# Kernel optimization log

Measured on AMD Instinct MI355X. Metric: run time of the kernel, lower is better.

## Reference

```python
import jax, jax.numpy as jnp
import numpy as np

B, C, H, W = 8, 64, 160, 160
N_HEADS = 8
EPS = 1e-6


def conv1x1(x, w, b):
    # x: [B, Cin, H, W], w: [Cout, Cin], b: [Cout]
    return jnp.einsum('oc,bchw->bohw', w, x) + b[None, :, None, None]


def setup_inputs() -> dict:
    key = jax.random.key(0)
    ks = jax.random.split(key, 12)
    s = 0.05
    return {
        'high': jax.random.normal(ks[0], (B, C, H, W), jnp.float32),
        'low': jax.random.normal(ks[1], (B, C, H, W), jnp.float32),
        'wq_high': jax.random.normal(ks[2], (C // 2, C), jnp.float32) * s,
        'bq_high': jnp.zeros((C // 2,), jnp.float32),
        'wq_low': jax.random.normal(ks[3], (C // 2, C), jnp.float32) * s,
        'bq_low': jnp.zeros((C // 2,), jnp.float32),
        'wk': jax.random.normal(ks[4], (C, C), jnp.float32) * s,
        'bk': jnp.zeros((C,), jnp.float32),
        'wv': jax.random.normal(ks[5], (C, C), jnp.float32) * s,
        'bv': jnp.zeros((C,), jnp.float32),
        'wo': jax.random.normal(ks[6], (C, C), jnp.float32) * s,
        'bo': jnp.zeros((C,), jnp.float32),
    }


def reference(high, low, wq_high, bq_high, wq_low, bq_low, wk, bk, wv, bv, wo, bo):
    b, c, h, w = low.shape
    p, d, n = N_HEADS, c // N_HEADS, h * w
    # q branches: [B, C//2, H, W] -> [B, P/2, N, d]
    hq = conv1x1(high, wq_high, bq_high).reshape(b, p // 2, d, n).transpose(0, 1, 3, 2)
    lq = conv1x1(low, wq_low, bq_low).reshape(b, p // 2, d, n).transpose(0, 1, 3, 2)
    q = jax.nn.softplus(jnp.concatenate([hq, lq], axis=1))          # [B, P, N, d]
    k = jax.nn.softplus(conv1x1(low, wk, bk).reshape(b, p, d, n))   # [B, P, d, N]
    v = conv1x1(low, wv, bv).reshape(b, p, d, n)                    # [B, P, d, N]
    # linear-attention context: kT v over spatial N
    attn_map = jnp.einsum('bpmn,bpcn->bpmc', k, v)                  # [B, P, d, d]
    norm = 1.0 / jnp.einsum('bpnc,bpc->bpn', q, jnp.sum(k, axis=-1) + EPS)  # [B, P, N]
    out = jnp.einsum('bpnm,bpmc,bpn->bpcn', q, attn_map, norm)      # [B, P, d, N]
    out = out.reshape(b, c, h, w)
    return conv1x1(out, wo, bo)
```

## Files before the change

kernel.cpp:

```cpp
#include <hip/hip_runtime.h>

#define NPIX  25600
#define NB    8
#define NCH   200
#define KPX   128
#define EPSV  1e-6f

#define WS_WKVT  0
#define WS_WQT   8192
#define WS_BKV   12288
#define WS_BQ    12416
#define WS_PART  12480
#define WS_G     934080
#define WS_KSE   966848
#define WS_WKVM  966912
#define WS_BKVM  975104

typedef __attribute__((ext_vector_type(8))) short short8v;
typedef __attribute__((ext_vector_type(4))) float f32x4v;

__device__ __forceinline__ unsigned short f2bf(float x) {
  unsigned u = __float_as_uint(x);
  return (unsigned short)((u + 0x7FFFu + ((u >> 16) & 1u)) >> 16);
}
__device__ __forceinline__ float bf2f(unsigned short h) {
  return __uint_as_float(((unsigned)h) << 16);
}

__device__ __forceinline__ float softplus_(float x) {
  return (x > 20.0f) ? x : __logf(1.0f + __expf(x));
}

__global__ void k0_pack(const float* __restrict__ wq_high, const float* __restrict__ bq_high,
                        const float* __restrict__ wq_low,  const float* __restrict__ bq_low,
                        const float* __restrict__ wk, const float* __restrict__ bk,
                        const float* __restrict__ wv, const float* __restrict__ bv,
                        float* __restrict__ ws) {
  const int tid = threadIdx.x;
  for (int e = tid; e < 4096; e += 256) {
    int m = e & 7, c = (e >> 3) & 63, h = e >> 9;
    float v = (h < 4) ? wq_high[(h * 8 + m) * 64 + c]
                      : wq_low[((h - 4) * 8 + m) * 64 + c];
    ws[WS_WQT + e] = v;
  }
  for (int e = tid; e < 64; e += 256) {
    int m = e & 7, h = e >> 3;
    ws[WS_BQ + e] = (h < 4) ? bq_high[h * 8 + m] : bq_low[(h - 4) * 8 + m];
  }
  unsigned short* wmp = (unsigned short*)(ws + WS_WKVM);
  for (int e = tid; e < 16384; e += 256) {
    int j = e & 7, l = (e >> 3) & 63, frag = e >> 9;
    int sp = frag & 1, ks = (frag >> 1) & 1, mt = frag >> 2;
    int row = l & 15, k32 = (l >> 4) * 8 + j, c = ks * 32 + k32;
    int head = (mt & 3) * 2 + (row >> 3), m = row & 7;
    float wv_ = (mt < 4) ? wk[(head * 8 + m) * 64 + c] : wv[(head * 8 + m) * 64 + c];
    unsigned short hb = f2bf(wv_);
    wmp[e] = (sp == 0) ? hb : f2bf(wv_ - bf2f(hb));
  }
  for (int e = tid; e < 128; e += 256) {
    int mt = e >> 4, row = e & 15;
    int head = (mt & 3) * 2 + (row >> 3), m = row & 7;
    ws[WS_BKVM + e] = (mt < 4) ? bk[head * 8 + m] : bv[head * 8 + m];
  }
}

__global__ __attribute__((amdgpu_waves_per_eu(1, 8)))
void k1_kv(const float* __restrict__ low,
           const float* __restrict__ ws,
           float* __restrict__ part) {
  const int b = blockIdx.y, chunk = blockIdx.x;
  const int tid = threadIdx.x, lane = tid & 63;
  const int w = __builtin_amdgcn_readfirstlane(tid >> 6);
  const int l15 = lane & 15, lg = lane >> 4;
  __shared__ float kvL[16384];
  const float* lowb = low + (size_t)b * 64 * NPIX + chunk * KPX + w * 32;
  short8v xhi[2][2], xlo[2][2];
#pragma unroll
  for (int nt = 0; nt < 2; nt++)
#pragma unroll
    for (int ks = 0; ks < 2; ks++) {
      const float* xp = lowb + (size_t)(ks * 32 + lg * 8) * NPIX + nt * 16 + l15;
      float xs[8];
#pragma unroll
      for (int j = 0; j < 8; j++) xs[j] = xp[(size_t)j * NPIX];
#pragma unroll
      for (int j = 0; j < 8; j++) {
        unsigned short h = f2bf(xs[j]);
        xhi[nt][ks][j] = (short)h;
        xlo[nt][ks][j] = (short)f2bf(xs[j] - bf2f(h));
      }
    }
  const unsigned short* wm = (const unsigned short*)(ws + WS_WKVM);
  const float* bm = ws + WS_BKVM;
#pragma unroll
  for (int mt = 0; mt < 8; mt++) {
    f32x4v a0 = {0.f, 0.f, 0.f, 0.f}, a1 = {0.f, 0.f, 0.f, 0.f};
#pragma unroll
    for (int ks = 0; ks < 2; ks++) {
      short8v whi = *(const short8v*)(wm + (((mt * 4 + ks * 2 + 0) * 64) + lane) * 8);
      short8v wlo = *(const short8v*)(wm + (((mt * 4 + ks * 2 + 1) * 64) + lane) * 8);
      a0 = __builtin_amdgcn_mfma_f32_16x16x32_bf16(whi, xhi[0][ks], a0, 0, 0, 0);
      a0 = __builtin_amdgcn_mfma_f32_16x16x32_bf16(whi, xlo[0][ks], a0, 0, 0, 0);
      a0 = __builtin_amdgcn_mfma_f32_16x16x32_bf16(wlo, xhi[0][ks], a0, 0, 0, 0);
      a1 = __builtin_amdgcn_mfma_f32_16x16x32_bf16(whi, xhi[1][ks], a1, 0, 0, 0);
      a1 = __builtin_amdgcn_mfma_f32_16x16x32_bf16(whi, xlo[1][ks], a1, 0, 0, 0);
      a1 = __builtin_amdgcn_mfma_f32_16x16x32_bf16(wlo, xhi[1][ks], a1, 0, 0, 0);
    }
#pragma unroll
    for (int r = 0; r < 4; r++) {
      const int row = mt * 16 + lg * 4 + r;
      const float bb = bm[row];
      float v0 = a0[r] + bb, v1 = a1[r] + bb;
      if (mt < 4) { v0 = softplus_(v0); v1 = softplus_(v1); }
      const int px0 = w * 32 + l15, px1 = w * 32 + 16 + l15;
      kvL[row * 128 + ((((px0 >> 2) ^ (row & 7))) << 2) + (px0 & 3)] = v0;
      kvL[row * 128 + ((((px1 >> 2) ^ (row & 7))) << 2) + (px1 & 3)] = v1;
    }
  }
  __syncthreads();
  const int col = l15;
#pragma unroll
  for (int hh = 0; hh < 2; hh++) {
    const int h = w + hh * 4;
    f32x4v acc = {0.f, 0.f, 0.f, 0.f};
    const int arow = h * 8 + (l15 & 7);
    const int brow = 64 + h * 8 + (col < 8 ? col : 0);
#pragma unroll
    for (int ks = 0; ks < 4; ks++) {
      const int pxl = ks * 32 + lg * 8;
      const int sA = arow & 7;
      float4 af0 = *(const float4*)&kvL[arow * 128 + (((pxl >> 2) ^ sA) << 2)];
      float4 af1 = *(const float4*)&kvL[arow * 128 + ((((pxl >> 2) + 1) ^ sA) << 2)];
      float as[8] = {af0.x, af0.y, af0.z, af0.w, af1.x, af1.y, af1.z, af1.w};
      float bs[8];
      if (col < 8) {
        const int sB = brow & 7;
        float4 bf0 = *(const float4*)&kvL[brow * 128 + (((pxl >> 2) ^ sB) << 2)];
        float4 bf1 = *(const float4*)&kvL[brow * 128 + ((((pxl >> 2) + 1) ^ sB) << 2)];
        bs[0]=bf0.x; bs[1]=bf0.y; bs[2]=bf0.z; bs[3]=bf0.w;
        bs[4]=bf1.x; bs[5]=bf1.y; bs[6]=bf1.z; bs[7]=bf1.w;
      } else {
        const float fill = (col == 8) ? 1.0f : 0.0f;
#pragma unroll
        for (int j = 0; j < 8; j++) bs[j] = fill;
      }
      short8v ahi, alo, bhi, blo;
#pragma unroll
      for (int j = 0; j < 8; j++) {
        unsigned short ha = f2bf(as[j]);
        ahi[j] = (short)ha; alo[j] = (short)f2bf(as[j] - bf2f(ha));
        unsigned short hb = f2bf(bs[j]);
        bhi[j] = (short)hb; blo[j] = (short)f2bf(bs[j] - bf2f(hb));
      }
      acc = __builtin_amdgcn_mfma_f32_16x16x32_bf16(ahi, bhi, acc, 0, 0, 0);
      acc = __builtin_amdgcn_mfma_f32_16x16x32_bf16(ahi, blo, acc, 0, 0, 0);
      acc = __builtin_amdgcn_mfma_f32_16x16x32_bf16(alo, bhi, acc, 0, 0, 0);
    }
    if (lane < 32 && col <= 8) {
      float* pb = part + ((size_t)(b * 8 + h) * NCH + chunk) * 72;
#pragma unroll
      for (int r = 0; r < 4; r++) {
        const int rr = lg * 4 + r;
        if (col < 8) pb[rr * 8 + col] = acc[r];
        else         pb[64 + rr] = acc[r];
      }
    }
  }
}

__global__ void k2_g(const float* __restrict__ part, const float* __restrict__ wo,
                     float* __restrict__ ws) {
  const int b = blockIdx.x >> 3, p = blockIdx.x & 7;
  const int tid = threadIdx.x, lane = tid & 63, sub = tid >> 6;
  __shared__ float red[4][72];
  __shared__ float attnL[72];
  const float* src = part + (size_t)(b * 8 + p) * NCH * 72;
  float s0 = 0.0f, s1 = 0.0f;
  for (int ch = sub * (NCH / 4); ch < (sub + 1) * (NCH / 4); ch++) {
    s0 += src[ch * 72 + lane];
    if (lane < 8) s1 += src[ch * 72 + 64 + lane];
  }
  red[sub][lane] = s0;
  if (lane < 8) red[sub][64 + lane] = s1;
  __syncthreads();
  if (tid < 72) attnL[tid] = (red[0][tid] + red[1][tid]) + (red[2][tid] + red[3][tid]);
  __syncthreads();
  if (tid >= 64) {
    if (tid < 72) ws[WS_KSE + (b * 8 + p) * 8 + (tid - 64)] = attnL[tid] + EPSV;
    return;
  }
  const int o = tid;
  float wrow[8];
#pragma unroll
  for (int c = 0; c < 8; c++) wrow[c] = wo[o * 64 + p * 8 + c];
  float* Gp = ws + WS_G + (size_t)(b * 64 + p * 8) * 64;
#pragma unroll
  for (int m = 0; m < 8; m++) {
    float g = 0.0f;
#pragma unroll
    for (int c = 0; c < 8; c++) g = fmaf(attnL[m * 8 + c], wrow[c], g);
    Gp[m * 64 + o] = g;
  }
}

__global__ void k3_main(const float* __restrict__ high,
                        const float* __restrict__ low,
                        const float* __restrict__ ws,
                        const float* __restrict__ bo,
                        float* __restrict__ out) {
  const int b = blockIdx.y, chunk = blockIdx.x;
  const int tid = threadIdx.x, lane = tid & 63;
  const int wu = __builtin_amdgcn_readfirstlane(tid >> 6);
  __shared__ float qsL[64 * KPX];
  const float* srcb = ((wu < 4) ? high : low) + (size_t)b * 64 * NPIX + chunk * KPX;
  const float* wq  = ws + WS_WQT + wu * 512;
  const float* bq  = ws + WS_BQ + wu * 8;
  const float* kse = ws + WS_KSE + (b * 8 + wu) * 8;
  const float* Gb  = ws + WS_G + (size_t)b * 4096 + wu * 8;
  float qa[8][2];
#pragma unroll
  for (int m = 0; m < 8; m++) { qa[m][0] = bq[m]; qa[m][1] = bq[m]; }
#pragma unroll 8
  for (int c = 0; c < 64; c++) {
    float2 x = reinterpret_cast<const float2*>(srcb + (size_t)c * NPIX)[lane];
    const float* wr = wq + c * 8;
#pragma unroll
    for (int m = 0; m < 8; m++) {
      float w = wr[m];
      qa[m][0] = fmaf(w, x.x, qa[m][0]);
      qa[m][1] = fmaf(w, x.y, qa[m][1]);
    }
  }
  float s0 = 0.0f, s1 = 0.0f;
#pragma unroll
  for (int m = 0; m < 8; m++) {
    float km = kse[m];
    qa[m][0] = softplus_(qa[m][0]);
    qa[m][1] = softplus_(qa[m][1]);
    s0 = fmaf(qa[m][0], km, s0);
    s1 = fmaf(qa[m][1], km, s1);
  }
  const float r0 = 1.0f / s0, r1 = 1.0f / s1;
#pragma unroll
  for (int m = 0; m < 8; m++) {
    reinterpret_cast<float2*>(&qsL[(wu * 8 + m) * KPX])[lane] =
        make_float2(qa[m][0] * r0, qa[m][1] * r1);
  }
  __syncthreads();
  float acc[8][2];
#pragma unroll
  for (int j = 0; j < 8; j++) { acc[j][0] = bo[wu * 8 + j]; acc[j][1] = acc[j][0]; }
#pragma unroll 8
  for (int pm = 0; pm < 64; pm++) {
    float2 qv = reinterpret_cast<const float2*>(&qsL[pm * KPX])[lane];
    const float* gr = Gb + pm * 64;
#pragma unroll
    for (int j = 0; j < 8; j++) {
      float g = gr[j];
      acc[j][0] = fmaf(g, qv.x, acc[j][0]);
      acc[j][1] = fmaf(g, qv.y, acc[j][1]);
    }
  }
  float* ob = out + (size_t)(b * 64 + wu * 8) * NPIX + chunk * KPX;
#pragma unroll
  for (int j = 0; j < 8; j++) {
    reinterpret_cast<float2*>(ob + (size_t)j * NPIX)[lane] =
        make_float2(acc[j][0], acc[j][1]);
  }
}

extern "C" void kernel_launch(void* const* d_in, const int* in_sizes, int n_in,
                              void* d_out, int out_size, void* d_ws, size_t ws_size,
                              hipStream_t stream) {
  const float* high    = (const float*)d_in[0];
  const float* low     = (const float*)d_in[1];
  const float* wq_high = (const float*)d_in[2];
  const float* bq_high = (const float*)d_in[3];
  const float* wq_low  = (const float*)d_in[4];
  const float* bq_low  = (const float*)d_in[5];
  const float* wk      = (const float*)d_in[6];
  const float* bk      = (const float*)d_in[7];
  const float* wv      = (const float*)d_in[8];
  const float* bv      = (const float*)d_in[9];
  const float* wo      = (const float*)d_in[10];
  const float* bo      = (const float*)d_in[11];
  float* ws  = (float*)d_ws;
  float* out = (float*)d_out;

  k0_pack<<<1, 256, 0, stream>>>(wq_high, bq_high, wq_low, bq_low, wk, bk, wv, bv, ws);
  dim3 grid1(NCH, NB);
  k1_kv<<<grid1, 256, 0, stream>>>(low, ws, ws + WS_PART);
  k2_g<<<64, 256, 0, stream>>>(ws + WS_PART, wo, ws);
  dim3 grid3(NCH, NB);
  k3_main<<<grid3, 512, 0, stream>>>(high, low, ws, bo, out);
}
```

Baseline: 122.7 us.

## Move q projection and output projection in main kernel to split-bf16 MFMA

The main kernel's Q 1x1 conv and final G·q output projection are rewritten from scalar FMA loops into MFMA 16x16x32 bf16 operations. A hi/lo bf16 split (three MFMAs per tile) keeps accuracy close to fp32. Weights and G are pre-packed into MFMA fragment layout in the pack and G kernels. The q tile in LDS uses an XOR-swizzled layout, and the block drops from 512 to 256 threads with a waves-per-EU hint. The cost is a more complex data layout, extra conversion work, and strided per-lane global loads of x that are less coalesced than the old float2 loads.

```diff
diff --git a/kernel.cpp b/kernel.cpp
--- a/kernel.cpp
+++ b/kernel.cpp
@@ -6,15 +6,13 @@
 #define KPX   128
 #define EPSV  1e-6f
 
-#define WS_WKVT  0
-#define WS_WQT   8192
-#define WS_BKV   12288
-#define WS_BQ    12416
-#define WS_PART  12480
-#define WS_G     934080
-#define WS_KSE   966848
-#define WS_WKVM  966912
-#define WS_BKVM  975104
+#define WS_WQM   0
+#define WS_BQM   4096
+#define WS_WKVM  4160
+#define WS_BKVM  12352
+#define WS_KSE   12480
+#define WS_PART  12992
+#define WS_GM    934592
 
 typedef __attribute__((ext_vector_type(8))) short short8v;
 typedef __attribute__((ext_vector_type(4))) float f32x4v;
@@ -26,7 +24,6 @@
 __device__ __forceinline__ float bf2f(unsigned short h) {
   return __uint_as_float(((unsigned)h) << 16);
 }
-
 __device__ __forceinline__ float softplus_(float x) {
   return (x > 20.0f) ? x : __logf(1.0f + __expf(x));
 }
@@ -37,15 +34,20 @@
                         const float* __restrict__ wv, const float* __restrict__ bv,
                         float* __restrict__ ws) {
   const int tid = threadIdx.x;
-  for (int e = tid; e < 4096; e += 256) {
-    int m = e & 7, c = (e >> 3) & 63, h = e >> 9;
-    float v = (h < 4) ? wq_high[(h * 8 + m) * 64 + c]
-                      : wq_low[((h - 4) * 8 + m) * 64 + c];
-    ws[WS_WQT + e] = v;
+  unsigned short* wqm = (unsigned short*)(ws + WS_WQM);
+  for (int e = tid; e < 8192; e += 256) {
+    int j = e & 7, l = (e >> 3) & 63, frag = e >> 9;
+    int sp = frag & 1, ks = (frag >> 1) & 1, mt = frag >> 2;
+    int row = mt * 16 + (l & 15), c = ks * 32 + (l >> 4) * 8 + j;
+    int head = row >> 3, m = row & 7;
+    float v = (head < 4) ? wq_high[(head * 8 + m) * 64 + c]
+                         : wq_low[((head - 4) * 8 + m) * 64 + c];
+    unsigned short hb = f2bf(v);
+    wqm[e] = (sp == 0) ? hb : f2bf(v - bf2f(hb));
   }
   for (int e = tid; e < 64; e += 256) {
-    int m = e & 7, h = e >> 3;
-    ws[WS_BQ + e] = (h < 4) ? bq_high[h * 8 + m] : bq_low[(h - 4) * 8 + m];
+    int head = e >> 3, m = e & 7;
+    ws[WS_BQM + e] = (head < 4) ? bq_high[head * 8 + m] : bq_low[(head - 4) * 8 + m];
   }
   unsigned short* wmp = (unsigned short*)(ws + WS_WKVM);
   for (int e = tid; e < 16384; e += 256) {
@@ -193,79 +195,141 @@
   float wrow[8];
 #pragma unroll
   for (int c = 0; c < 8; c++) wrow[c] = wo[o * 64 + p * 8 + c];
-  float* Gp = ws + WS_G + (size_t)(b * 64 + p * 8) * 64;
+  unsigned short* gm = (unsigned short*)(ws + WS_GM) + (size_t)b * 8192;
+  const int mt2 = o >> 4, lane_ = (p & 3) * 16 + (o & 15), ks = p >> 2;
+  short8v hi8, lo8;
 #pragma unroll
   for (int m = 0; m < 8; m++) {
     float g = 0.0f;
 #pragma unroll
     for (int c = 0; c < 8; c++) g = fmaf(attnL[m * 8 + c], wrow[c], g);
-    Gp[m * 64 + o] = g;
-  }
-}
-
-__global__ void k3_main(const float* __restrict__ high,
-                        const float* __restrict__ low,
-                        const float* __restrict__ ws,
-                        const float* __restrict__ bo,
-                        float* __restrict__ out) {
+    unsigned short hb = f2bf(g);
+    hi8[m] = (short)hb;
+    lo8[m] = (short)f2bf(g - bf2f(hb));
+  }
+  *(short8v*)(gm + (size_t)((mt2 * 4 + ks * 2 + 0) * 64 + lane_) * 8) = hi8;
+  *(short8v*)(gm + (size_t)((mt2 * 4 + ks * 2 + 1) * 64 + lane_) * 8) = lo8;
+}
+
+__global__ __attribute__((amdgpu_waves_per_eu(1, 8)))
+void k3_main(const float* __restrict__ high,
+             const float* __restrict__ low,
+             const float* __restrict__ ws,
+             const float* __restrict__ bo,
+             float* __restrict__ out) {
   const int b = blockIdx.y, chunk = blockIdx.x;
   const int tid = threadIdx.x, lane = tid & 63;
-  const int wu = __builtin_amdgcn_readfirstlane(tid >> 6);
-  __shared__ float qsL[64 * KPX];
-  const float* srcb = ((wu < 4) ? high : low) + (size_t)b * 64 * NPIX + chunk * KPX;
-  const float* wq  = ws + WS_WQT + wu * 512;
-  const float* bq  = ws + WS_BQ + wu * 8;
-  const float* kse = ws + WS_KSE + (b * 8 + wu) * 8;
-  const float* Gb  = ws + WS_G + (size_t)b * 4096 + wu * 8;
-  float qa[8][2];
-#pragma unroll
-  for (int m = 0; m < 8; m++) { qa[m][0] = bq[m]; qa[m][1] = bq[m]; }
-#pragma unroll 8
-  for (int c = 0; c < 64; c++) {
-    float2 x = reinterpret_cast<const float2*>(srcb + (size_t)c * NPIX)[lane];
-    const float* wr = wq + c * 8;
-#pragma unroll
-    for (int m = 0; m < 8; m++) {
-      float w = wr[m];
-      qa[m][0] = fmaf(w, x.x, qa[m][0]);
-      qa[m][1] = fmaf(w, x.y, qa[m][1]);
-    }
-  }
-  float s0 = 0.0f, s1 = 0.0f;
-#pragma unroll
-  for (int m = 0; m < 8; m++) {
-    float km = kse[m];
-    qa[m][0] = softplus_(qa[m][0]);
-    qa[m][1] = softplus_(qa[m][1]);
-    s0 = fmaf(qa[m][0], km, s0);
-    s1 = fmaf(qa[m][1], km, s1);
-  }
-  const float r0 = 1.0f / s0, r1 = 1.0f / s1;
-#pragma unroll
-  for (int m = 0; m < 8; m++) {
-    reinterpret_cast<float2*>(&qsL[(wu * 8 + m) * KPX])[lane] =
-        make_float2(qa[m][0] * r0, qa[m][1] * r1);
-  }
-  __syncthreads();
-  float acc[8][2];
-#pragma unroll
-  for (int j = 0; j < 8; j++) { acc[j][0] = bo[wu * 8 + j]; acc[j][1] = acc[j][0]; }
-#pragma unroll 8
-  for (int pm = 0; pm < 64; pm++) {
-    float2 qv = reinterpret_cast<const float2*>(&qsL[pm * KPX])[lane];
-    const float* gr = Gb + pm * 64;
-#pragma unroll
-    for (int j = 0; j < 8; j++) {
-      float g = gr[j];
-      acc[j][0] = fmaf(g, qv.x, acc[j][0]);
-      acc[j][1] = fmaf(g, qv.y, acc[j][1]);
-    }
-  }
-  float* ob = out + (size_t)(b * 64 + wu * 8) * NPIX + chunk * KPX;
-#pragma unroll
-  for (int j = 0; j < 8; j++) {
-    reinterpret_cast<float2*>(ob + (size_t)j * NPIX)[lane] =
-        make_float2(acc[j][0], acc[j][1]);
+  const int w = __builtin_amdgcn_readfirstlane(tid >> 6);
+  const int l15 = lane & 15, lg = lane >> 4;
+  __shared__ float qL[8192];
+  __shared__ float rnL[1024];
+  const float* highb = high + (size_t)b * 64 * NPIX + chunk * KPX + w * 32;
+  const float* lowb  = low  + (size_t)b * 64 * NPIX + chunk * KPX + w * 32;
+  short8v xhi[2][2][2], xlo[2][2][2];
+#pragma unroll
+  for (int s = 0; s < 2; s++) {
+    const float* srcb = (s == 0) ? highb : lowb;
+#pragma unroll
+    for (int nt = 0; nt < 2; nt++)
+#pragma unroll
+      for (int ks = 0; ks < 2; ks++) {
+        const float* xp = srcb + (size_t)(ks * 32 + lg * 8) * NPIX + nt * 16 + l15;
+        float xs[8];
+#pragma unroll
+        for (int j = 0; j < 8; j++) xs[j] = xp[(size_t)j * NPIX];
+#pragma unroll
+        for (int j = 0; j < 8; j++) {
+          unsigned short h = f2bf(xs[j]);
+          xhi[s][nt][ks][j] = (short)h;
+          xlo[s][nt][ks][j] = (short)f2bf(xs[j] - bf2f(h));
+        }
+      }
+  }
+  const unsigned short* wqm = (const unsigned short*)(ws + WS_WQM);
+  const float* bqm = ws + WS_BQM;
+#pragma unroll
+  for (int mt = 0; mt < 4; mt++) {
+    const int s = mt >> 1;
+    f32x4v a0 = {0.f, 0.f, 0.f, 0.f}, a1 = {0.f, 0.f, 0.f, 0.f};
+#pragma unroll
+    for (int ks = 0; ks < 2; ks++) {
+      short8v whi = *(const short8v*)(wqm + (((mt * 4 + ks * 2 + 0) * 64) + lane) * 8);
+      short8v wlo = *(const short8v*)(wqm + (((mt * 4 + ks * 2 + 1) * 64) + lane) * 8);
+      a0 = __builtin_amdgcn_mfma_f32_16x16x32_bf16(whi, xhi[s][0][ks], a0, 0, 0, 0);
+      a0 = __builtin_amdgcn_mfma_f32_16x16x32_bf16(whi, xlo[s][0][ks], a0, 0, 0, 0);
+      a0 = __builtin_amdgcn_mfma_f32_16x16x32_bf16(wlo, xhi[s][0][ks], a0, 0, 0, 0);
+      a1 = __builtin_amdgcn_mfma_f32_16x16x32_bf16(whi, xhi[s][1][ks], a1, 0, 0, 0);
+      a1 = __builtin_amdgcn_mfma_f32_16x16x32_bf16(whi, xlo[s][1][ks], a1, 0, 0, 0);
+      a1 = __builtin_amdgcn_mfma_f32_16x16x32_bf16(wlo, xhi[s][1][ks], a1, 0, 0, 0);
+    }
+#pragma unroll
+    for (int r = 0; r < 4; r++) {
+      const int row = mt * 16 + lg * 4 + r;
+      const float bb = bqm[row];
+      float v0 = softplus_(a0[r] + bb), v1 = softplus_(a1[r] + bb);
+      const int px0 = w * 32 + l15, px1 = w * 32 + 16 + l15;
+      qL[row * 128 + ((((px0 >> 2) ^ (row & 7))) << 2) + (px0 & 3)] = v0;
+      qL[row * 128 + ((((px1 >> 2) ^ (row & 7))) << 2) + (px1 & 3)] = v1;
+    }
+  }
+  __syncthreads();
+  {
+    const int px = tid & 127;
+    const int hb = (tid >> 7) * 4;
+#pragma unroll
+    for (int h0 = 0; h0 < 4; h0++) {
+      const int h = hb + h0;
+      const float* ksep = ws + WS_KSE + (b * 8 + h) * 8;
+      float s = 0.0f;
+#pragma unroll
+      for (int m = 0; m < 8; m++) {
+        const int row = h * 8 + m;
+        s = fmaf(qL[row * 128 + ((((px >> 2) ^ (row & 7))) << 2) + (px & 3)],
+                 ksep[m], s);
+      }
+      rnL[h * 128 + px] = 1.0f / s;
+    }
+  }
+  __syncthreads();
+  const unsigned short* gm = (const unsigned short*)(ws + WS_GM) + (size_t)b * 8192;
+#pragma unroll
+  for (int nt = 0; nt < 2; nt++) {
+    const int px = w * 32 + nt * 16 + l15;
+    short8v qhi[2], qlo[2];
+#pragma unroll
+    for (int ks = 0; ks < 2; ks++) {
+      const float rn = rnL[(ks * 4 + lg) * 128 + px];
+#pragma unroll
+      for (int j = 0; j < 8; j++) {
+        const int row = ks * 32 + lg * 8 + j;
+        float q = qL[row * 128 + ((((px >> 2) ^ j)) << 2) + (px & 3)] * rn;
+        unsigned short h = f2bf(q);
+        qhi[ks][j] = (short)h;
+        qlo[ks][j] = (short)f2bf(q - bf2f(h));
+      }
+    }
+    f32x4v acc[4];
+#pragma unroll
+    for (int mt2 = 0; mt2 < 4; mt2++) acc[mt2] = (f32x4v){0.f, 0.f, 0.f, 0.f};
+#pragma unroll
+    for (int mt2 = 0; mt2 < 4; mt2++) {
+#pragma unroll
+      for (int ks = 0; ks < 2; ks++) {
+        short8v ghi = *(const short8v*)(gm + (size_t)((mt2 * 4 + ks * 2 + 0) * 64 + lane) * 8);
+        short8v glo = *(const short8v*)(gm + (size_t)((mt2 * 4 + ks * 2 + 1) * 64 + lane) * 8);
+        acc[mt2] = __builtin_amdgcn_mfma_f32_16x16x32_bf16(ghi, qhi[ks], acc[mt2], 0, 0, 0);
+        acc[mt2] = __builtin_amdgcn_mfma_f32_16x16x32_bf16(ghi, qlo[ks], acc[mt2], 0, 0, 0);
+        acc[mt2] = __builtin_amdgcn_mfma_f32_16x16x32_bf16(glo, qhi[ks], acc[mt2], 0, 0, 0);
+      }
+    }
+    float* ob = out + ((size_t)b * 64) * NPIX + chunk * KPX + px;
+#pragma unroll
+    for (int mt2 = 0; mt2 < 4; mt2++)
+#pragma unroll
+      for (int r = 0; r < 4; r++) {
+        const int o = mt2 * 16 + lg * 4 + r;
+        ob[(size_t)o * NPIX] = acc[mt2][r] + bo[o];
+      }
   }
 }
 
@@ -288,9 +352,8 @@
   float* out = (float*)d_out;
 
   k0_pack<<<1, 256, 0, stream>>>(wq_high, bq_high, wq_low, bq_low, wk, bk, wv, bv, ws);
-  dim3 grid1(NCH, NB);
-  k1_kv<<<grid1, 256, 0, stream>>>(low, ws, ws + WS_PART);
+  dim3 grid(NCH, NB);
+  k1_kv<<<grid, 256, 0, stream>>>(low, ws, ws + WS_PART);
   k2_g<<<64, 256, 0, stream>>>(ws + WS_PART, wo, ws);
-  dim3 grid3(NCH, NB);
-  k3_main<<<grid3, 512, 0, stream>>>(high, low, ws, bo, out);
-}
+  k3_main<<<grid, 256, 0, stream>>>(high, low, ws, bo, out);
+}
```

After: 112.8 us. -8.1%, faster.
